# Performance work log

Hardware: AMD Instinct MI355X
Metric: run time of the kernel (lower is better)

The kernel has to match this reference:

```python
import jax, jax.numpy as jnp
import numpy as np

B, T, N, F_OUT, K, HID = 8, 12, 4096, 12, 3, 64
HALF = T // 2


def setup_inputs() -> dict:
    key = jax.random.key(0)
    ks = jax.random.split(key, 7)
    return {
        "x": jax.random.normal(ks[0], (B, T, N, 1), jnp.float32),
        "adj": jax.random.normal(ks[1], (K, N, N), jnp.float32) / np.float32(np.sqrt(N)),
        "cheb_w": jax.random.normal(ks[2], (HID, K), jnp.float32) / np.float32(np.sqrt(K)),
        "gcn_w": jax.random.normal(ks[3], (F_OUT, T, 1, HID), jnp.float32) / np.float32(np.sqrt(T * HID)),
        "gcn_b": jnp.zeros((F_OUT,), jnp.float32),
        "glu1_w": jax.random.normal(ks[4], (F_OUT, HALF, 3, 3), jnp.float32) / np.float32(np.sqrt(HALF * 9)),
        "glu1_b": jnp.zeros((F_OUT,), jnp.float32),
        "glu2_w": jax.random.normal(ks[5], (F_OUT, HALF, 3, 3), jnp.float32) / np.float32(np.sqrt(HALF * 9)),
        "glu2_b": jnp.zeros((F_OUT,), jnp.float32),
    }


def _dilated_conv(x, w, b):
    # Conv2d(kernel=3, dilation=2, padding=2) on (B, C, N, 1)
    y = jax.lax.conv_general_dilated(
        x, w, window_strides=(1, 1), padding=((2, 2), (2, 2)),
        rhs_dilation=(2, 2), dimension_numbers=("NCHW", "OIHW", "NCHW"))
    return y + b[None, :, None, None]


def reference(x, adj, cheb_w, gcn_w, gcn_b, glu1_w, glu1_b, glu2_w, glu2_b):
    # --- ChebConv (vectorized over the per-channel Python loop) ---
    # x: (B, T, N, 1), adj: (K, N, N) -> y: (B, T, N, K)
    y = jnp.einsum("knm,btm->btnk", adj, x[..., 0])
    # Linear(K -> HID, no bias) + ReLU -> cheb: (B, T, N, HID)
    cheb = jax.nn.relu(jnp.einsum("btnk,ok->btno", y, cheb_w))
    # --- gcn_conv: Conv2d(T -> F_OUT, kernel (1, HID)) -> (B, F_OUT, N, 1) ---
    sgc = jnp.einsum("btnj,otj->bon", cheb, gcn_w[:, :, 0, :]) + gcn_b[None, :, None]
    sgc = sgc[..., None]
    # --- GLU path: split history in half, dilated convs, a * sigmoid(g) ---
    x_u, x_v = x[:, :HALF], x[:, HALF:]
    a = _dilated_conv(x_u, glu1_w, glu1_b)
    g = _dilated_conv(x_v, glu2_w, glu2_b)
    x_glu = a * jax.nn.sigmoid(g)
    return x_glu + sgc
```

## Files before the change

### kernel.cpp

```cpp
#include <hip/hip_runtime.h>
#include <hip/hip_bf16.h>
#include <math.h>

#define NNODES 4096
#define NCOLS  96
#define NROWS  12288
#define KSEG   16
#define KLEN   (NNODES / KSEG)
#define NST    (KLEN / 32)

typedef __attribute__((ext_vector_type(8))) short short8;
typedef __attribute__((ext_vector_type(4))) float float4v;

__global__ void probe_dtype(const unsigned int* __restrict__ aw, int* __restrict__ flag) {
    int tid = threadIdx.x;
    unsigned w = aw[tid];
    unsigned e = (w >> 7) & 0xffu;
    bool insane = (e >= 0xC0u) || (e <= 0x30u);
    unsigned long long m = __ballot(insane);
    if (tid == 0) flag[0] = (__popcll(m) >= 16) ? 1 : 0;
}

__device__ __forceinline__ float ldf(const void* p, size_t i, int isf32) {
    return isf32 ? ((const float*)p)[i]
                 : __bfloat162float(((const __hip_bfloat16*)p)[i]);
}

__device__ __forceinline__ void ld8(float* d, const void* p, size_t e, int isf32) {
    if (isf32) {
        const float4* s = (const float4*)((const float*)p + e);
        float4 f0 = s[0], f1 = s[1];
        d[0] = f0.x; d[1] = f0.y; d[2] = f0.z; d[3] = f0.w;
        d[4] = f1.x; d[5] = f1.y; d[6] = f1.z; d[7] = f1.w;
    } else {
        const __hip_bfloat16* s = (const __hip_bfloat16*)p + e;
#pragma unroll
        for (int j = 0; j < 8; j++) d[j] = __bfloat162float(s[j]);
    }
}

__device__ __forceinline__ short8 cvt8(float4 a, float4 b) {
    union { short8 v; __hip_bfloat16 h[8]; } u;
    u.h[0] = __float2bfloat16(a.x); u.h[1] = __float2bfloat16(a.y);
    u.h[2] = __float2bfloat16(a.z); u.h[3] = __float2bfloat16(a.w);
    u.h[4] = __float2bfloat16(b.x); u.h[5] = __float2bfloat16(b.y);
    u.h[6] = __float2bfloat16(b.z); u.h[7] = __float2bfloat16(b.w);
    return u.v;
}

__global__ __launch_bounds__(256) void cvt_x(
    const void* __restrict__ xv, __hip_bfloat16* __restrict__ xbf,
    const int* __restrict__ flag)
{
    const int isf32 = flag[0];
    const int i = (blockIdx.x * 256 + threadIdx.x) * 8;
    if (isf32) {
        const float* xf = (const float*)xv;
        float4 f0 = *(const float4*)(xf + i);
        float4 f1 = *(const float4*)(xf + i + 4);
        short8 v = cvt8(f0, f1);
        *(short8*)(xbf + i) = v;
    } else {
        *(uint4*)(xbf + i) = *(const uint4*)((const __hip_bfloat16*)xv + i);
    }
}

__global__ __launch_bounds__(512, 4) void gemm_y(
    const void* __restrict__ adjv, const __hip_bfloat16* __restrict__ xbf,
    float* __restrict__ yws, const int* __restrict__ flag)
{
    __shared__ uint4 Xs[96 * 32];

    const int tid = threadIdx.x;
    const int isf32 = flag[0];
    const int wv = tid >> 6, ln = tid & 63, fr = ln & 15, fq = ln >> 4;

    const int bid = blockIdx.x;
    const int rt0 = (bid >> 4) * 128;
    const int ks  = bid & 15;
    const int k0  = ks * KLEN;

#pragma unroll
    for (int s = 0; s < 6; s++) {
        int L = tid + s * 512;
        int r = L >> 5, c = L & 31;
        Xs[r * 32 + (c ^ (r & 7))] =
            *(const uint4*)(xbf + (size_t)r * NNODES + k0 + c * 8);
    }

    float4v acc[6];
#pragma unroll
    for (int i = 0; i < 6; i++) acc[i] = (float4v){0.f, 0.f, 0.f, 0.f};

    const int arow = rt0 + wv * 16 + fr;
    __syncthreads();

#define XFRAG(CT, STEP) \
    (*(const short8*)&Xs[((CT) * 16 + fr) * 32 + ((((STEP) * 4) + fq) ^ (((CT) * 16 + fr) & 7))])

    if (isf32) {
        const float* ap = (const float*)adjv + (size_t)arow * NNODES + k0 + fq * 8;
        float4 AA[2], AB[2];

#define ALOADF(R, STEP) { const float* p = ap + (STEP) * 32;                   \
        R[0] = *(const float4*)p; R[1] = *(const float4*)(p + 4); }
#define COMPF(R, STEP) { short8 a = cvt8(R[0], R[1]);                          \
        _Pragma("unroll")                                                      \
        for (int ct = 0; ct < 6; ct++)                                         \
            acc[ct] = __builtin_amdgcn_mfma_f32_16x16x32_bf16(a, XFRAG(ct, STEP), acc[ct], 0, 0, 0); }

        ALOADF(AA, 0); ALOADF(AB, 1);
        COMPF(AA, 0);  ALOADF(AA, 2);
        COMPF(AB, 1);  ALOADF(AB, 3);
        COMPF(AA, 2);  ALOADF(AA, 4);
        COMPF(AB, 3);  ALOADF(AB, 5);
        COMPF(AA, 4);  ALOADF(AA, 6);
        COMPF(AB, 5);  ALOADF(AB, 7);
        COMPF(AA, 6);
        COMPF(AB, 7);
#undef ALOADF
#undef COMPF
    } else {
        const __hip_bfloat16* ap = (const __hip_bfloat16*)adjv + (size_t)arow * NNODES + k0 + fq * 8;
        uint4 AA, AB;

#define ALOADB(R, STEP) R = *(const uint4*)(ap + (STEP) * 32);
#define COMPB(R, STEP) { short8 a = *(const short8*)&R;                        \
        _Pragma("unroll")                                                      \
        for (int ct = 0; ct < 6; ct++)                                         \
            acc[ct] = __builtin_amdgcn_mfma_f32_16x16x32_bf16(a, XFRAG(ct, STEP), acc[ct], 0, 0, 0); }

        ALOADB(AA, 0); ALOADB(AB, 1);
        COMPB(AA, 0);  ALOADB(AA, 2);
        COMPB(AB, 1);  ALOADB(AB, 3);
        COMPB(AA, 2);  ALOADB(AA, 4);
        COMPB(AB, 3);  ALOADB(AB, 5);
        COMPB(AA, 4);  ALOADB(AA, 6);
        COMPB(AB, 5);  ALOADB(AB, 7);
        COMPB(AA, 6);
        COMPB(AB, 7);
#undef ALOADB
#undef COMPB
    }
#undef XFRAG

    float* yo = yws + (size_t)ks * NROWS * NCOLS;
#pragma unroll
    for (int ct = 0; ct < 6; ct++)
#pragma unroll
        for (int rg = 0; rg < 4; rg++) {
            size_t r = (size_t)rt0 + wv * 16 + fq * 4 + rg;
            yo[r * NCOLS + ct * 16 + fr] = acc[ct][rg];
        }
}

__global__ __launch_bounds__(256) void epilogue_kernel(
    const void* __restrict__ xv, const float* __restrict__ yws,
    const void* __restrict__ chebv, const void* __restrict__ gcnwv,
    const void* __restrict__ gcnbv, const void* __restrict__ g1wv,
    const void* __restrict__ g1bv, const void* __restrict__ g2wv,
    const void* __restrict__ g2bv,
    float* __restrict__ out, const int* __restrict__ flag)
{
    __shared__ float gwL[9216];
    __shared__ float cwL[192];
    __shared__ float w1L[216];
    __shared__ float w2L[216];
    __shared__ float wbL[36];

    const int tid = threadIdx.x;
    const int isf32 = flag[0];

    for (int i = tid; i < 9216; i += 256) {
        int o = i / 768, t = (i / 64) % 12, j = i % 64;
        gwL[t * 768 + j * 12 + o] = ldf(gcnwv, i, isf32);
    }
    if (tid < 192) cwL[tid] = ldf(chebv, tid, isf32);
    if (tid < 216) {
        w1L[tid] = ldf(g1wv, (size_t)tid * 3 + 1, isf32);
        w2L[tid] = ldf(g2wv, (size_t)tid * 3 + 1, isf32);
    }
    if (tid < 12) {
        wbL[tid]      = ldf(gcnbv, tid, isf32);
        wbL[12 + tid] = ldf(g1bv, tid, isf32);
        wbL[24 + tid] = ldf(g2bv, tid, isf32);
    }
    __syncthreads();

    const int gid = blockIdx.x * 256 + tid;
    const int pr  = gid >> 2;
    const int tq  = gid & 3;
    const int b = pr >> 12;
    const int n = pr & (NNODES - 1);

    float yk[3][3];
#pragma unroll
    for (int k = 0; k < 3; k++) { yk[k][0] = 0.f; yk[k][1] = 0.f; yk[k][2] = 0.f; }
#pragma unroll 4
    for (int s = 0; s < KSEG; s++) {
        const float* base = yws + (size_t)s * NROWS * NCOLS;
#pragma unroll
        for (int k = 0; k < 3; k++) {
            const float* yp = base + ((size_t)(k * NNODES + n)) * NCOLS + b * 12 + tq * 3;
            yk[k][0] += yp[0]; yk[k][1] += yp[1]; yk[k][2] += yp[2];
        }
    }

    float sg[12];
#pragma unroll
    for (int o = 0; o < 12; o++) sg[o] = 0.f;
#pragma unroll
    for (int i = 0; i < 3; i++) {
        const float y0 = yk[0][i], y1 = yk[1][i], y2 = yk[2][i];
        const float* gwt = gwL + (tq * 3 + i) * 768;
#pragma unroll 4
        for (int j = 0; j < 64; j++) {
            float h = y0 * cwL[j * 3] + y1 * cwL[j * 3 + 1] + y2 * cwL[j * 3 + 2];
            h = fmaxf(h, 0.f);
#pragma unroll
            for (int o = 0; o < 12; o++) sg[o] += h * gwt[j * 12 + o];
        }
    }
#pragma unroll
    for (int o = 0; o < 12; o++) {
        sg[o] += __shfl_xor(sg[o], 1);
        sg[o] += __shfl_xor(sg[o], 2);
    }

    float xa[18], xg[18];
#pragma unroll
    for (int c = 0; c < 6; c++)
#pragma unroll
        for (int kh = 0; kh < 3; kh++) {
            int m = n + 2 * kh - 2;
            bool ok = ((unsigned)m < (unsigned)NNODES);
            xa[c * 3 + kh] = ok ? ldf(xv, ((size_t)(b * 12 + c)) * NNODES + m, isf32) : 0.f;
            xg[c * 3 + kh] = ok ? ldf(xv, ((size_t)(b * 12 + c + 6)) * NNODES + m, isf32) : 0.f;
        }

#pragma unroll
    for (int i = 0; i < 3; i++) {
        const int o = tq * 3 + i;
        float av = wbL[12 + o], gv = wbL[24 + o];
#pragma unroll
        for (int q = 0; q < 18; q++) {
            av += xa[q] * w1L[o * 18 + q];
            gv += xg[q] * w2L[o * 18 + q];
        }
        float s = 1.f / (1.f + expf(-gv));
        out[((size_t)(b * 12 + o)) * NNODES + n] = av * s + sg[o] + wbL[o];
    }
}

__global__ __launch_bounds__(64) void fused_simple(
    const void* __restrict__ xv, const void* __restrict__ adjv,
    const void* __restrict__ chebv, const void* __restrict__ gcnwv,
    const void* __restrict__ gcnbv, const void* __restrict__ g1wv,
    const void* __restrict__ g1bv, const void* __restrict__ g2wv,
    const void* __restrict__ g2bv,
    float* __restrict__ out, const int* __restrict__ flag)
{
    __shared__ float gwL[9216];
    __shared__ float cwL[192];
    __shared__ float w1L[216];
    __shared__ float w2L[216];
    __shared__ float wbL[36];

    const int tid = threadIdx.x;
    const int isf32 = flag[0];

    for (int i = tid; i < 9216; i += 64) {
        int o = i / 768, t = (i / 64) % 12, j = i % 64;
        gwL[t * 768 + j * 12 + o] = ldf(gcnwv, i, isf32);
    }
    for (int i = tid; i < 192; i += 64) cwL[i] = ldf(chebv, i, isf32);
    for (int i = tid; i < 216; i += 64) {
        w1L[i] = ldf(g1wv, (size_t)i * 3 + 1, isf32);
        w2L[i] = ldf(g2wv, (size_t)i * 3 + 1, isf32);
    }
    if (tid < 12) {
        wbL[tid]      = ldf(gcnbv, tid, isf32);
        wbL[12 + tid] = ldf(g1bv, tid, isf32);
        wbL[24 + tid] = ldf(g2bv, tid, isf32);
    }
    __syncthreads();

    const int g = blockIdx.x * 64 + tid;
    const int b = g >> 12;
    const int n = g & (NNODES - 1);

    float y[3][12];
#pragma unroll
    for (int k = 0; k < 3; k++)
#pragma unroll
        for (int t = 0; t < 12; t++) y[k][t] = 0.f;

    for (int m0 = 0; m0 < NNODES; m0 += 8) {
        float a0[8], a1[8], a2[8];
        ld8(a0, adjv, ((size_t)(0 * NNODES + n)) * NNODES + m0, isf32);
        ld8(a1, adjv, ((size_t)(1 * NNODES + n)) * NNODES + m0, isf32);
        ld8(a2, adjv, ((size_t)(2 * NNODES + n)) * NNODES + m0, isf32);
#pragma unroll
        for (int t = 0; t < 12; t++) {
            float x8[8];
            ld8(x8, xv, ((size_t)(b * 12 + t)) * NNODES + m0, isf32);
#pragma unroll
            for (int j = 0; j < 8; j++) {
                y[0][t] += a0[j] * x8[j];
                y[1][t] += a1[j] * x8[j];
                y[2][t] += a2[j] * x8[j];
            }
        }
    }

    float sg[12];
#pragma unroll
    for (int o = 0; o < 12; o++) sg[o] = wbL[o];
    for (int t = 0; t < 12; t++) {
        const float y0 = y[0][t], y1 = y[1][t], y2 = y[2][t];
        const float* gwt = gwL + t * 768;
#pragma unroll 4
        for (int j = 0; j < 64; j++) {
            float h = y0 * cwL[j * 3] + y1 * cwL[j * 3 + 1] + y2 * cwL[j * 3 + 2];
            h = fmaxf(h, 0.f);
#pragma unroll
            for (int o = 0; o < 12; o++) sg[o] += h * gwt[j * 12 + o];
        }
    }

    float xa[18], xg[18];
#pragma unroll
    for (int c = 0; c < 6; c++)
#pragma unroll
        for (int kh = 0; kh < 3; kh++) {
            int m = n + 2 * kh - 2;
            bool ok = ((unsigned)m < (unsigned)NNODES);
            xa[c * 3 + kh] = ok ? ldf(xv, ((size_t)(b * 12 + c)) * NNODES + m, isf32) : 0.f;
            xg[c * 3 + kh] = ok ? ldf(xv, ((size_t)(b * 12 + c + 6)) * NNODES + m, isf32) : 0.f;
        }

#pragma unroll
    for (int o = 0; o < 12; o++) {
        float av = wbL[12 + o], gv = wbL[24 + o];
#pragma unroll
        for (int i = 0; i < 18; i++) {
            av += xa[i] * w1L[o * 18 + i];
            gv += xg[i] * w2L[o * 18 + i];
        }
        float s = 1.f / (1.f + expf(-gv));
        out[((size_t)(b * 12 + o)) * NNODES + n] = av * s + sg[o];
    }
}

extern "C" void kernel_launch(void* const* d_in, const int* in_sizes, int n_in,
                              void* d_out, int out_size, void* d_ws, size_t ws_size,
                              hipStream_t stream)
{
    int* flag = (int*)d_ws;
    __hip_bfloat16* xbf = (__hip_bfloat16*)((char*)d_ws + 64);
    float* yws = (float*)((char*)d_ws + 64 + (size_t)NCOLS * NNODES * 2);
    const size_t need = 64 + (size_t)NCOLS * NNODES * 2
                      + (size_t)KSEG * NROWS * NCOLS * 4;

    hipLaunchKernelGGL(probe_dtype, dim3(1), dim3(64), 0, stream,
                       (const unsigned int*)d_in[1], flag);

    if (ws_size >= need) {
        hipLaunchKernelGGL(cvt_x, dim3(192), dim3(256), 0, stream,
                           d_in[0], xbf, flag);
        hipLaunchKernelGGL(gemm_y, dim3(96 * KSEG), dim3(512), 0, stream,
                           d_in[1], xbf, yws, flag);
        hipLaunchKernelGGL(epilogue_kernel, dim3(512), dim3(256), 0, stream,
                           d_in[0], yws, d_in[2], d_in[3], d_in[4],
                           d_in[5], d_in[6], d_in[7], d_in[8],
                           (float*)d_out, flag);
    } else {
        hipLaunchKernelGGL(fused_simple, dim3(512), dim3(64), 0, stream,
                           d_in[0], d_in[1], d_in[2], d_in[3], d_in[4],
                           d_in[5], d_in[6], d_in[7], d_in[8],
                           (float*)d_out, flag);
    }
}
```

Measured before the change: 375.9 us.

## Inline dtype probe, add coalesced split-K reduce kernel, vectorize epilogue weights

Drops the separate probe launch: each kernel now recomputes the fp32-vs-bf16 flag from the first 64 words of adj. Adds a reduce_y kernel that sums the 16 split-K partial slices with coalesced float4 loads, so the epilogue reads a single reduced slice instead of doing strided scalar gathers across all slices. The epilogue's Chebyshev and GCN weights are padded so they can be read as float4 from shared memory, and gemm_y's barrier moves after the first A loads to overlap them with the X tile staging. The cost is one extra kernel launch plus a full pass over the partial-sum workspace.

After: 380.8 us. No clear change (+1.3%).

```diff
diff --git a/kernel.cpp b/kernel.cpp
--- a/kernel.cpp
+++ b/kernel.cpp
@@ -7,18 +7,17 @@
 #define NROWS  12288
 #define KSEG   16
 #define KLEN   (NNODES / KSEG)
-#define NST    (KLEN / 32)
 
 typedef __attribute__((ext_vector_type(8))) short short8;
 typedef __attribute__((ext_vector_type(4))) float float4v;
 
-__global__ void probe_dtype(const unsigned int* __restrict__ aw, int* __restrict__ flag) {
-    int tid = threadIdx.x;
-    unsigned w = aw[tid];
+__device__ __forceinline__ int probe32(const void* adjp) {
+    const unsigned* aw = (const unsigned*)adjp;
+    unsigned w = aw[threadIdx.x & 63];
     unsigned e = (w >> 7) & 0xffu;
     bool insane = (e >= 0xC0u) || (e <= 0x30u);
     unsigned long long m = __ballot(insane);
-    if (tid == 0) flag[0] = (__popcll(m) >= 16) ? 1 : 0;
+    return (__popcll(m) >= 16) ? 1 : 0;
 }
 
 __device__ __forceinline__ float ldf(const void* p, size_t i, int isf32) {
@@ -50,9 +49,9 @@
 
 __global__ __launch_bounds__(256) void cvt_x(
     const void* __restrict__ xv, __hip_bfloat16* __restrict__ xbf,
-    const int* __restrict__ flag)
-{
-    const int isf32 = flag[0];
+    const void* __restrict__ adjp)
+{
+    const int isf32 = probe32(adjp);
     const int i = (blockIdx.x * 256 + threadIdx.x) * 8;
     if (isf32) {
         const float* xf = (const float*)xv;
@@ -67,12 +66,12 @@
 
 __global__ __launch_bounds__(512, 4) void gemm_y(
     const void* __restrict__ adjv, const __hip_bfloat16* __restrict__ xbf,
-    float* __restrict__ yws, const int* __restrict__ flag)
+    float* __restrict__ yws)
 {
     __shared__ uint4 Xs[96 * 32];
 
     const int tid = threadIdx.x;
-    const int isf32 = flag[0];
+    const int isf32 = probe32(adjv);
     const int wv = tid >> 6, ln = tid & 63, fr = ln & 15, fq = ln >> 4;
 
     const int bid = blockIdx.x;
@@ -93,7 +92,6 @@
     for (int i = 0; i < 6; i++) acc[i] = (float4v){0.f, 0.f, 0.f, 0.f};
 
     const int arow = rt0 + wv * 16 + fr;
-    __syncthreads();
 
 #define XFRAG(CT, STEP) \
     (*(const short8*)&Xs[((CT) * 16 + fr) * 32 + ((((STEP) * 4) + fq) ^ (((CT) * 16 + fr) & 7))])
@@ -110,6 +108,7 @@
             acc[ct] = __builtin_amdgcn_mfma_f32_16x16x32_bf16(a, XFRAG(ct, STEP), acc[ct], 0, 0, 0); }
 
         ALOADF(AA, 0); ALOADF(AB, 1);
+        __syncthreads();
         COMPF(AA, 0);  ALOADF(AA, 2);
         COMPF(AB, 1);  ALOADF(AB, 3);
         COMPF(AA, 2);  ALOADF(AA, 4);
@@ -131,6 +130,7 @@
             acc[ct] = __builtin_amdgcn_mfma_f32_16x16x32_bf16(a, XFRAG(ct, STEP), acc[ct], 0, 0, 0); }
 
         ALOADB(AA, 0); ALOADB(AB, 1);
+        __syncthreads();
         COMPB(AA, 0);  ALOADB(AA, 2);
         COMPB(AB, 1);  ALOADB(AB, 3);
         COMPB(AA, 2);  ALOADB(AA, 4);
@@ -154,28 +154,43 @@
         }
 }
 
+__global__ __launch_bounds__(256) void reduce_y(float* __restrict__ yws)
+{
+    const size_t i = ((size_t)blockIdx.x * 256 + threadIdx.x) * 4;
+    float4 s = *(const float4*)(yws + i);
+#pragma unroll
+    for (int sl = 1; sl < KSEG; sl++) {
+        const float4 v = *(const float4*)(yws + (size_t)sl * NROWS * NCOLS + i);
+        s.x += v.x; s.y += v.y; s.z += v.z; s.w += v.w;
+    }
+    *(float4*)(yws + i) = s;
+}
+
 __global__ __launch_bounds__(256) void epilogue_kernel(
     const void* __restrict__ xv, const float* __restrict__ yws,
     const void* __restrict__ chebv, const void* __restrict__ gcnwv,
     const void* __restrict__ gcnbv, const void* __restrict__ g1wv,
     const void* __restrict__ g1bv, const void* __restrict__ g2wv,
     const void* __restrict__ g2bv,
-    float* __restrict__ out, const int* __restrict__ flag)
-{
-    __shared__ float gwL[9216];
-    __shared__ float cwL[192];
+    float* __restrict__ out, const void* __restrict__ adjp)
+{
+    __shared__ __align__(16) float gwL[9216];
+    __shared__ __align__(16) float cw4L[256];
     __shared__ float w1L[216];
     __shared__ float w2L[216];
     __shared__ float wbL[36];
 
     const int tid = threadIdx.x;
-    const int isf32 = flag[0];
+    const int isf32 = probe32(adjp);
 
     for (int i = tid; i < 9216; i += 256) {
         int o = i / 768, t = (i / 64) % 12, j = i % 64;
         gwL[t * 768 + j * 12 + o] = ldf(gcnwv, i, isf32);
     }
-    if (tid < 192) cwL[tid] = ldf(chebv, tid, isf32);
+    if (tid < 256) {
+        int j = tid >> 2, kk = tid & 3;
+        cw4L[tid] = (kk < 3 && j < 64) ? ldf(chebv, j * 3 + kk, isf32) : 0.f;
+    }
     if (tid < 216) {
         w1L[tid] = ldf(g1wv, (size_t)tid * 3 + 1, isf32);
         w2L[tid] = ldf(g2wv, (size_t)tid * 3 + 1, isf32);
@@ -195,30 +210,28 @@
 
     float yk[3][3];
 #pragma unroll
-    for (int k = 0; k < 3; k++) { yk[k][0] = 0.f; yk[k][1] = 0.f; yk[k][2] = 0.f; }
-#pragma unroll 4
-    for (int s = 0; s < KSEG; s++) {
-        const float* base = yws + (size_t)s * NROWS * NCOLS;
-#pragma unroll
-        for (int k = 0; k < 3; k++) {
-            const float* yp = base + ((size_t)(k * NNODES + n)) * NCOLS + b * 12 + tq * 3;
-            yk[k][0] += yp[0]; yk[k][1] += yp[1]; yk[k][2] += yp[2];
-        }
+    for (int k = 0; k < 3; k++) {
+        const float* yp = yws + ((size_t)(k * NNODES + n)) * NCOLS + b * 12 + tq * 3;
+        yk[k][0] = yp[0]; yk[k][1] = yp[1]; yk[k][2] = yp[2];
     }
 
     float sg[12];
 #pragma unroll
     for (int o = 0; o < 12; o++) sg[o] = 0.f;
+    const float4* cw4 = (const float4*)cw4L;
 #pragma unroll
     for (int i = 0; i < 3; i++) {
         const float y0 = yk[0][i], y1 = yk[1][i], y2 = yk[2][i];
-        const float* gwt = gwL + (tq * 3 + i) * 768;
+        const float4* gw4 = (const float4*)(gwL + (tq * 3 + i) * 768);
 #pragma unroll 4
         for (int j = 0; j < 64; j++) {
-            float h = y0 * cwL[j * 3] + y1 * cwL[j * 3 + 1] + y2 * cwL[j * 3 + 2];
+            float4 cw = cw4[j];
+            float h = fmaf(y0, cw.x, fmaf(y1, cw.y, y2 * cw.z));
             h = fmaxf(h, 0.f);
-#pragma unroll
-            for (int o = 0; o < 12; o++) sg[o] += h * gwt[j * 12 + o];
+            float4 g0 = gw4[j * 3], g1 = gw4[j * 3 + 1], g2 = gw4[j * 3 + 2];
+            sg[0] += h * g0.x; sg[1] += h * g0.y; sg[2]  += h * g0.z; sg[3]  += h * g0.w;
+            sg[4] += h * g1.x; sg[5] += h * g1.y; sg[6]  += h * g1.z; sg[7]  += h * g1.w;
+            sg[8] += h * g2.x; sg[9] += h * g2.y; sg[10] += h * g2.z; sg[11] += h * g2.w;
         }
     }
 #pragma unroll
@@ -258,7 +271,7 @@
     const void* __restrict__ gcnbv, const void* __restrict__ g1wv,
     const void* __restrict__ g1bv, const void* __restrict__ g2wv,
     const void* __restrict__ g2bv,
-    float* __restrict__ out, const int* __restrict__ flag)
+    float* __restrict__ out)
 {
     __shared__ float gwL[9216];
     __shared__ float cwL[192];
@@ -267,7 +280,7 @@
     __shared__ float wbL[36];
 
     const int tid = threadIdx.x;
-    const int isf32 = flag[0];
+    const int isf32 = probe32(adjv);
 
     for (int i = tid; i < 9216; i += 64) {
         int o = i / 768, t = (i / 64) % 12, j = i % 64;
@@ -356,28 +369,26 @@
                               void* d_out, int out_size, void* d_ws, size_t ws_size,
                               hipStream_t stream)
 {
-    int* flag = (int*)d_ws;
     __hip_bfloat16* xbf = (__hip_bfloat16*)((char*)d_ws + 64);
     float* yws = (float*)((char*)d_ws + 64 + (size_t)NCOLS * NNODES * 2);
     const size_t need = 64 + (size_t)NCOLS * NNODES * 2
                       + (size_t)KSEG * NROWS * NCOLS * 4;
 
-    hipLaunchKernelGGL(probe_dtype, dim3(1), dim3(64), 0, stream,
-                       (const unsigned int*)d_in[1], flag);
-
     if (ws_size >= need) {
         hipLaunchKernelGGL(cvt_x, dim3(192), dim3(256), 0, stream,
-                           d_in[0], xbf, flag);
+                           d_in[0], xbf, d_in[1]);
         hipLaunchKernelGGL(gemm_y, dim3(96 * KSEG), dim3(512), 0, stream,
-                           d_in[1], xbf, yws, flag);
+                           d_in[1], xbf, yws);
+        hipLaunchKernelGGL(reduce_y, dim3(NROWS * NCOLS / 1024), dim3(256), 0, stream,
+                           yws);
         hipLaunchKernelGGL(epilogue_kernel, dim3(512), dim3(256), 0, stream,
                            d_in[0], yws, d_in[2], d_in[3], d_in[4],
                            d_in[5], d_in[6], d_in[7], d_in[8],
-                           (float*)d_out, flag);
+                           (float*)d_out, d_in[1]);
     } else {
         hipLaunchKernelGGL(fused_simple, dim3(512), dim3(64), 0, stream,
                            d_in[0], d_in[1], d_in[2], d_in[3], d_in[4],
                            d_in[5], d_in[6], d_in[7], d_in[8],
-                           (float*)d_out, flag);
-    }
-}
+                           (float*)d_out);
+    }
+}
```
